# Optimization experiments

Hardware: AMD Instinct MI355X
Metric: run time of the kernel (lower is better)

Reference implementation:

```python
import jax, jax.numpy as jnp
import numpy as np

NUM_BINS = 10
NUM_CLASSES = 128
ALPHA = 0.999
LABEL_SMOOTHING = 0.0


def setup_inputs() -> dict:
    key = jax.random.key(0)
    k1, k2, k3 = jax.random.split(key, 3)
    B, T, C = 16, 4096, NUM_CLASSES
    return {
        "pred_logits": jax.random.normal(k1, (B, T, C), dtype=jnp.float32),
        "target_prob": jax.random.uniform(k2, (B, T, C), dtype=jnp.float32),
        "mask": jax.random.uniform(k3, (B, T, 1), dtype=jnp.float32),
        "GD_stat_ema": jnp.ones((NUM_BINS,), dtype=jnp.float32),
        "label_stat_ema_each_class": jnp.ones((NUM_CLASSES * 3,), dtype=jnp.float32),
    }


def _bce_with_logits(x, t):
    # numerically stable BCEWithLogitsLoss, reduction='none'
    return jnp.maximum(x, 0.0) - x * t + jnp.log1p(jnp.exp(-jnp.abs(x)))


def _update_ema(ema, hist, num_bins):
    hist = hist / jnp.maximum(hist.sum(), 1e-10) * num_bins
    ema = ema * ALPHA + (1.0 - ALPHA) * hist
    return ema / jnp.maximum(ema.sum(), 1e-10) * num_bins


def reference(pred_logits, target_prob, mask, GD_stat_ema, label_stat_ema_each_class):
    m = jnp.broadcast_to(mask, pred_logits.shape)
    tp = jnp.clip(target_prob, LABEL_SMOOTHING, 1.0 - LABEL_SMOOTHING)

    raw_loss = _bce_with_logits(pred_logits, tp)
    pred_prob = jax.nn.sigmoid(pred_logits)
    grad_mag = jnp.abs(pred_prob - tp)

    bin_idx = jnp.clip(jnp.floor(grad_mag * NUM_BINS).astype(jnp.int32), 0, NUM_BINS - 1)
    GD_weights = 1.0 / jax.lax.stop_gradient(GD_stat_ema[bin_idx])

    # per-class 3-way probability bin: idx in [0, 3*num_classes)
    tpi = jnp.clip(jnp.floor(tp * 3.0).astype(jnp.int32), 0, 2) + 3 * jnp.arange(NUM_CLASSES, dtype=jnp.int32)
    classes_weights = 1.0 / jax.lax.stop_gradient(label_stat_ema_each_class[tpi])

    weights = jnp.sqrt(GD_weights * classes_weights)
    loss = (raw_loss * weights * m).sum() / jnp.maximum(m.sum(), 1e-10)

    # weighted histograms (bincount with float weights)
    GD_hist = jnp.zeros((NUM_BINS,), dtype=jnp.float32).at[bin_idx.ravel()].add(m.ravel())
    label_hist = jnp.zeros((NUM_CLASSES * 3,), dtype=jnp.float32).at[tpi.ravel()].add(m.ravel())

    GD_ema_new = _update_ema(GD_stat_ema, GD_hist, NUM_BINS)
    label_ema_new = _update_ema(label_stat_ema_each_class, label_hist, NUM_CLASSES * 3)
    return loss, GD_ema_new, label_ema_new
```

## Files before the change

kernel.cpp:

```cpp
#include <hip/hip_runtime.h>

#define NBINS 10
#define LBINS 384
#define NOUT  395
#define PSTRIDE 400
#define PQ (PSTRIDE / 4)
#define BLOCK 256

typedef float f32x4 __attribute__((ext_vector_type(4)));

#define SGRID 1024
#define OUTER 2
#define BATCH 4
#define SGSTR (SGRID * BLOCK)

__global__ __launch_bounds__(256) void ghm_main_s(
    const float* __restrict__ xg, const float* __restrict__ tg,
    const float* __restrict__ mask,
    const float* __restrict__ gd_ema, const float* __restrict__ lab_ema,
    float* __restrict__ ws)
{
    __shared__ float s_rsgd[NBINS];
    __shared__ float s_rslab[LBINS];
    __shared__ float s_out[PSTRIDE];
    __shared__ float s_red[4];

    const int tid = threadIdx.x;
    if (tid < NBINS) s_rsgd[tid] = __builtin_amdgcn_rsqf(gd_ema[tid]);
    for (int i = tid; i < LBINS; i += BLOCK) s_rslab[i] = __builtin_amdgcn_rsqf(lab_ema[i]);
    for (int i = tid; i < PSTRIDE; i += BLOCK) s_out[i] = 0.f;
    __syncthreads();

    const int c0 = (tid & 31) * 4;
    float wl[4][3];
#pragma unroll
    for (int j = 0; j < 4; ++j)
#pragma unroll
        for (int t = 0; t < 3; ++t) wl[j][t] = s_rslab[(c0 + j) * 3 + t];

    float lab[4][3] = {{0.f}};
    float gdl[NBINS];
#pragma unroll
    for (int b = 0; b < NBINS; ++b) gdl[b] = 0.f;
    float loss_acc = 0.f;

    const f32x4* x4 = (const f32x4*)xg;
    const f32x4* t4 = (const f32x4*)tg;
    const int i0 = blockIdx.x * BLOCK + tid;

#pragma unroll
    for (int o = 0; o < OUTER; ++o) {
        f32x4 xv[BATCH], tv[BATCH]; float mv[BATCH];
#pragma unroll
        for (int k = 0; k < BATCH; ++k) {
            const int i = i0 + (o * BATCH + k) * SGSTR;
            xv[k] = __builtin_nontemporal_load(&x4[i]);
            tv[k] = __builtin_nontemporal_load(&t4[i]);
            mv[k] = __builtin_nontemporal_load(&mask[i >> 5]);
        }
#pragma unroll
        for (int k = 0; k < BATCH; ++k) {
            const float m = mv[k];
            const float xs[4] = {xv[k].x, xv[k].y, xv[k].z, xv[k].w};
            const float ts[4] = {tv[k].x, tv[k].y, tv[k].z, tv[k].w};
            unsigned pack = 0u;
#pragma unroll
            for (int j = 0; j < 4; ++j) {
                const float x  = xs[j];
                const float tp = ts[j];
                const float E  = __expf(-fabsf(x));
                const float z  = 1.f + E;
                const float raw = fmaxf(x, 0.f) - x * tp + __logf(z);
                const float inv = __builtin_amdgcn_rcpf(z);
                const float tps = (x >= 0.f) ? tp : 1.f - tp;
                const float g   = fabsf(inv - tps);
                int bin = (int)(g * 10.f);  bin = bin > 9 ? 9 : bin;
                int t3  = (int)(tp * 3.f);  t3  = t3 > 2 ? 2 : t3;
                const float wlj = (t3 == 0) ? wl[j][0] : ((t3 == 1) ? wl[j][1] : wl[j][2]);
                const float w = s_rsgd[bin] * wlj;
                loss_acc = fmaf(raw * m, w, loss_acc);
#pragma unroll
                for (int t = 0; t < 3; ++t) lab[j][t] += (t3 == t) ? m : 0.f;
                pack += 1u << (3 * bin);
            }
#pragma unroll
            for (int b = 0; b < NBINS; ++b)
                gdl[b] = fmaf(m, (float)((pack >> (3 * b)) & 7u), gdl[b]);
        }
    }

    const int lane = tid & 63, wv = tid >> 6;
    float v = loss_acc;
#pragma unroll
    for (int off = 32; off > 0; off >>= 1) v += __shfl_down(v, off);
    if (lane == 0) s_red[wv] = v;
#pragma unroll
    for (int b = 0; b < NBINS; ++b) {
        float g = gdl[b];
#pragma unroll
        for (int off = 32; off > 0; off >>= 1) g += __shfl_down(g, off);
        if (lane == 0) atomicAdd(&s_out[1 + b], g);
    }
#pragma unroll
    for (int j = 0; j < 4; ++j)
#pragma unroll
        for (int t = 0; t < 3; ++t)
            atomicAdd(&s_out[11 + (c0 + j) * 3 + t], lab[j][t]);
    __syncthreads();

    float* slot = ws + (size_t)blockIdx.x * PSTRIDE;
    if (tid == 0) slot[0] = s_red[0] + s_red[1] + s_red[2] + s_red[3];
    if (tid >= 1) slot[tid] = s_out[tid];
    if (tid < PSTRIDE - BLOCK) slot[BLOCK + tid] = s_out[BLOCK + tid];
}

__global__ __launch_bounds__(256) void ghm_fin1(
    const float* __restrict__ ws, float* __restrict__ ws2, int nrows)
{
    __shared__ float4 r[BLOCK];
    const int tid = threadIdx.x;
    const float4* p = (const float4*)ws + blockIdx.x;
    float4 a = make_float4(0.f, 0.f, 0.f, 0.f);
    for (int b = tid; b < nrows; b += BLOCK) {
        float4 u = p[(size_t)b * PQ];
        a.x += u.x; a.y += u.y; a.z += u.z; a.w += u.w;
    }
    r[tid] = a;
    __syncthreads();
    for (int off = BLOCK / 2; off > 0; off >>= 1) {
        if (tid < off) {
            float4 u = r[tid + off];
            r[tid].x += u.x; r[tid].y += u.y; r[tid].z += u.z; r[tid].w += u.w;
        }
        __syncthreads();
    }
    if (tid == 0) ((float4*)ws2)[blockIdx.x] = r[0];
}

__global__ __launch_bounds__(512) void ghm_fin2(
    const float* __restrict__ sv_g,
    const float* __restrict__ gd_ema, const float* __restrict__ lab_ema,
    float* __restrict__ out)
{
    __shared__ float sv[PSTRIDE];
    __shared__ float red[512];
    __shared__ float s_sc[1];

    const int tid = threadIdx.x;
    if (tid < PSTRIDE) sv[tid] = sv_g[tid];
    __syncthreads();

    if (tid == 0) {
        float ms = 0.f;
        for (int b = 0; b < NBINS; ++b) ms += sv[1 + b];
        const float inv_m = 1.f / fmaxf(ms, 1e-10f);
        s_sc[0] = inv_m;
        out[0] = sv[0] * inv_m;
        float ge[NBINS], gs = 0.f;
        for (int b = 0; b < NBINS; ++b) {
            ge[b] = gd_ema[b] * 0.999f + 0.001f * (sv[1 + b] * inv_m * (float)NBINS);
            gs += ge[b];
        }
        const float ig = 1.f / fmaxf(gs, 1e-10f);
        for (int b = 0; b < NBINS; ++b) out[1 + b] = ge[b] * ig * (float)NBINS;
    }
    __syncthreads();
    const float inv_m = s_sc[0];

    float e = 0.f;
    if (tid < LBINS)
        e = lab_ema[tid] * 0.999f + 0.001f * (sv[11 + tid] * inv_m * (float)LBINS);
    red[tid] = e;
    __syncthreads();
    for (int off = 256; off > 0; off >>= 1) {
        if (tid < off) red[tid] += red[tid + off];
        __syncthreads();
    }
    const float ie = (float)LBINS / fmaxf(red[0], 1e-10f);
    if (tid < LBINS) out[11 + tid] = e * ie;
}

#define NSLICE 8
#define SLICE_STRIDE 512
#define AGRID 2048
#define AITER 4
#define AGSTR (AGRID * BLOCK)

__global__ __launch_bounds__(256) void ghm_main_a(
    const float* __restrict__ xg, const float* __restrict__ tg,
    const float* __restrict__ mask,
    const float* __restrict__ gd_ema, const float* __restrict__ lab_ema,
    float* __restrict__ ws)
{
    __shared__ float s_rsgd[NBINS];
    __shared__ float s_rslab[LBINS];
    __shared__ float s_hlab[LBINS];
    __shared__ float s_hgd[NBINS];
    __shared__ float s_red[4];

    const int tid = threadIdx.x;
    if (tid < NBINS) { s_rsgd[tid] = __builtin_amdgcn_rsqf(gd_ema[tid]); s_hgd[tid] = 0.f; }
    for (int i = tid; i < LBINS; i += BLOCK) {
        s_rslab[i] = __builtin_amdgcn_rsqf(lab_ema[i]);
        s_hlab[i]  = 0.f;
    }
    __syncthreads();

    const int c0 = (tid & 31) * 4;
    float wl[4][3];
#pragma unroll
    for (int j = 0; j < 4; ++j)
#pragma unroll
        for (int t = 0; t < 3; ++t) wl[j][t] = s_rslab[(c0 + j) * 3 + t];

    float lab[4][3] = {{0.f}};
    float gdl[NBINS];
#pragma unroll
    for (int b = 0; b < NBINS; ++b) gdl[b] = 0.f;
    float loss_acc = 0.f;

    const float4* x4 = (const float4*)xg;
    const float4* t4 = (const float4*)tg;
    const int i0 = blockIdx.x * BLOCK + tid;

    float4 xv[AITER], tv[AITER]; float mv[AITER];
#pragma unroll
    for (int k = 0; k < AITER; ++k) {
        const int i = i0 + k * AGSTR;
        xv[k] = x4[i]; tv[k] = t4[i]; mv[k] = mask[i >> 5];
    }
#pragma unroll
    for (int k = 0; k < AITER; ++k) {
        const float m = mv[k];
        const float xs[4] = {xv[k].x, xv[k].y, xv[k].z, xv[k].w};
        const float ts[4] = {tv[k].x, tv[k].y, tv[k].z, tv[k].w};
        unsigned pack = 0u;
#pragma unroll
        for (int j = 0; j < 4; ++j) {
            const float x  = xs[j];
            const float tp = ts[j];
            const float E  = __expf(-fabsf(x));
            const float z  = 1.f + E;
            const float raw = fmaxf(x, 0.f) - x * tp + __logf(z);
            const float inv = __builtin_amdgcn_rcpf(z);
            const float tps = (x >= 0.f) ? tp : 1.f - tp;
            const float g   = fabsf(inv - tps);
            int bin = (int)(g * 10.f);  bin = bin > 9 ? 9 : bin;
            int t3  = (int)(tp * 3.f);  t3  = t3 > 2 ? 2 : t3;
            const float wlj = (t3 == 0) ? wl[j][0] : ((t3 == 1) ? wl[j][1] : wl[j][2]);
            const float w = s_rsgd[bin] * wlj;
            loss_acc = fmaf(raw * m, w, loss_acc);
#pragma unroll
            for (int t = 0; t < 3; ++t) lab[j][t] += (t3 == t) ? m : 0.f;
            pack += 1u << (3 * bin);
        }
#pragma unroll
        for (int b = 0; b < NBINS; ++b)
            gdl[b] = fmaf(m, (float)((pack >> (3 * b)) & 7u), gdl[b]);
    }

    const int lane = tid & 63, wv = tid >> 6;
    float v = loss_acc;
#pragma unroll
    for (int off = 32; off > 0; off >>= 1) v += __shfl_down(v, off);
    if (lane == 0) s_red[wv] = v;
#pragma unroll
    for (int b = 0; b < NBINS; ++b) {
        float g = gdl[b];
#pragma unroll
        for (int off = 32; off > 0; off >>= 1) g += __shfl_down(g, off);
        if (lane == 0) atomicAdd(&s_hgd[b], g);
    }
#pragma unroll
    for (int j = 0; j < 4; ++j)
#pragma unroll
        for (int t = 0; t < 3; ++t)
            atomicAdd(&s_hlab[(c0 + j) * 3 + t], lab[j][t]);
    __syncthreads();

    float* wss = ws + (blockIdx.x & (NSLICE - 1)) * SLICE_STRIDE;
    if (tid == 0) atomicAdd(&wss[0], s_red[0] + s_red[1] + s_red[2] + s_red[3]);
    if (tid < NBINS) atomicAdd(&wss[1 + tid], s_hgd[tid]);
    for (int e = tid; e < LBINS; e += BLOCK) atomicAdd(&wss[1 + NBINS + e], s_hlab[e]);
}

__global__ __launch_bounds__(512) void ghm_fin_a(
    const float* __restrict__ ws,
    const float* __restrict__ gd_ema, const float* __restrict__ lab_ema,
    float* __restrict__ out)
{
    __shared__ float red[512];
    __shared__ float s_gde[NBINS];
    __shared__ float s_gesum;

    const int tid = threadIdx.x;
    float v = 0.f;
    if (tid < NOUT) {
#pragma unroll
        for (int s = 0; s < NSLICE; ++s) v += ws[s * SLICE_STRIDE + tid];
    }
    red[tid] = (tid >= 1 && tid < 1 + NBINS) ? v : 0.f;
    __syncthreads();
    for (int off = 256; off > 0; off >>= 1) {
        if (tid < off) red[tid] += red[tid + off];
        __syncthreads();
    }
    const float msum = red[0];
    __syncthreads();
    const float inv_m = 1.f / fmaxf(msum, 1e-10f);
    if (tid == 0) out[0] = v * inv_m;
    if (tid >= 1 && tid < 1 + NBINS) {
        float hn = v * inv_m * (float)NBINS;
        s_gde[tid - 1] = gd_ema[tid - 1] * 0.999f + 0.001f * hn;
    }
    __syncthreads();
    if (tid == 0) {
        float s = 0.f;
        for (int b = 0; b < NBINS; ++b) s += s_gde[b];
        s_gesum = s;
    }
    __syncthreads();
    if (tid >= 1 && tid < 1 + NBINS)
        out[tid] = s_gde[tid - 1] / fmaxf(s_gesum, 1e-10f) * (float)NBINS;

    float e = 0.f;
    if (tid >= 1 + NBINS && tid < NOUT) {
        float hn = v * inv_m * (float)LBINS;
        e = lab_ema[tid - 1 - NBINS] * 0.999f + 0.001f * hn;
    }
    red[tid] = e;
    __syncthreads();
    for (int off = 256; off > 0; off >>= 1) {
        if (tid < off) red[tid] += red[tid + off];
        __syncthreads();
    }
    const float esum = red[0];
    if (tid >= 1 + NBINS && tid < NOUT)
        out[tid] = e / fmaxf(esum, 1e-10f) * (float)LBINS;
}

extern "C" void kernel_launch(void* const* d_in, const int* in_sizes, int n_in,
                              void* d_out, int out_size, void* d_ws, size_t ws_size,
                              hipStream_t stream)
{
    const float* logits  = (const float*)d_in[0];
    const float* tprob   = (const float*)d_in[1];
    const float* mask    = (const float*)d_in[2];
    const float* gd_ema  = (const float*)d_in[3];
    const float* lab_ema = (const float*)d_in[4];
    float* out = (float*)d_out;
    float* ws  = (float*)d_ws;

    const size_t need_s = ((size_t)SGRID * PSTRIDE + PSTRIDE) * sizeof(float);
    if (ws_size >= need_s) {
        float* ws2 = ws + (size_t)SGRID * PSTRIDE;
        ghm_main_s<<<SGRID, BLOCK, 0, stream>>>(logits, tprob, mask, gd_ema, lab_ema, ws);
        ghm_fin1<<<PQ, BLOCK, 0, stream>>>(ws, ws2, SGRID);
        ghm_fin2<<<1, 512, 0, stream>>>(ws2, gd_ema, lab_ema, out);
    } else {
        hipMemsetAsync(ws, 0, NSLICE * SLICE_STRIDE * sizeof(float), stream);
        ghm_main_a<<<AGRID, BLOCK, 0, stream>>>(logits, tprob, mask, gd_ema, lab_ema, ws);
        ghm_fin_a<<<1, 512, 0, stream>>>(ws, gd_ema, lab_ema, out);
    }
}
```

Before: 142.3 us.

## Stream inputs through LDS with direct global-to-LDS loads and staged waits

The main kernel now issues all eight iterations' logits and target loads up front as global_load_lds transfers into a 64KB per-block LDS pipeline buffer. Each stage waits on a decreasing vmcnt so compute on early tiles overlaps the remaining loads. The per-element math is factored into a shared helper that the fallback kernel also uses. The large LDS allocation lowers occupancy, and the nontemporal load hints are dropped.

```diff
diff --git a/kernel.cpp b/kernel.cpp
--- a/kernel.cpp
+++ b/kernel.cpp
@@ -9,12 +9,45 @@
 
 typedef float f32x4 __attribute__((ext_vector_type(4)));
 
+#define TO_LDS(p) ((__attribute__((address_space(3))) void*)(uintptr_t)(p))
+#define TO_GLB(p) ((const __attribute__((address_space(1))) void*)(uintptr_t)(p))
+
 #define SGRID 1024
-#define OUTER 2
-#define BATCH 4
 #define SGSTR (SGRID * BLOCK)
 
-__global__ __launch_bounds__(256) void ghm_main_s(
+__device__ __forceinline__ void ghm_elem4(
+    const f32x4 xv, const f32x4 tv, const float m,
+    const float wl[4][3], const float* s_rsgd,
+    float lab[4][3], float gdl[NBINS], float& loss_acc)
+{
+    const float xs[4] = {xv.x, xv.y, xv.z, xv.w};
+    const float ts[4] = {tv.x, tv.y, tv.z, tv.w};
+    unsigned pack = 0u;
+#pragma unroll
+    for (int j = 0; j < 4; ++j) {
+        const float x  = xs[j];
+        const float tp = ts[j];
+        const float E  = __expf(-fabsf(x));
+        const float z  = 1.f + E;
+        const float raw = fmaxf(x, 0.f) - x * tp + __logf(z);
+        const float inv = __builtin_amdgcn_rcpf(z);
+        const float tps = (x >= 0.f) ? tp : 1.f - tp;
+        const float g   = fabsf(inv - tps);
+        int bin = (int)(g * 10.f);  bin = bin > 9 ? 9 : bin;
+        int t3  = (int)(tp * 3.f);  t3  = t3 > 2 ? 2 : t3;
+        const float wlj = (t3 == 0) ? wl[j][0] : ((t3 == 1) ? wl[j][1] : wl[j][2]);
+        const float w = s_rsgd[bin] * wlj;
+        loss_acc = fmaf(raw * m, w, loss_acc);
+#pragma unroll
+        for (int t = 0; t < 3; ++t) lab[j][t] += (t3 == t) ? m : 0.f;
+        pack += 1u << (3 * bin);
+    }
+#pragma unroll
+    for (int b = 0; b < NBINS; ++b)
+        gdl[b] = fmaf(m, (float)((pack >> (3 * b)) & 7u), gdl[b]);
+}
+
+__global__ __launch_bounds__(256) void ghm_main_l(
     const float* __restrict__ xg, const float* __restrict__ tg,
     const float* __restrict__ mask,
     const float* __restrict__ gd_ema, const float* __restrict__ lab_ema,
@@ -24,6 +57,7 @@
     __shared__ float s_rslab[LBINS];
     __shared__ float s_out[PSTRIDE];
     __shared__ float s_red[4];
+    __shared__ __align__(16) float s_pipe[4][8][2][256];
 
     const int tid = threadIdx.x;
     if (tid < NBINS) s_rsgd[tid] = __builtin_amdgcn_rsqf(gd_ema[tid]);
@@ -46,50 +80,33 @@
 
     const f32x4* x4 = (const f32x4*)xg;
     const f32x4* t4 = (const f32x4*)tg;
+    const int lane = tid & 63, wv = tid >> 6;
     const int i0 = blockIdx.x * BLOCK + tid;
 
-#pragma unroll
-    for (int o = 0; o < OUTER; ++o) {
-        f32x4 xv[BATCH], tv[BATCH]; float mv[BATCH];
-#pragma unroll
-        for (int k = 0; k < BATCH; ++k) {
-            const int i = i0 + (o * BATCH + k) * SGSTR;
-            xv[k] = __builtin_nontemporal_load(&x4[i]);
-            tv[k] = __builtin_nontemporal_load(&t4[i]);
-            mv[k] = __builtin_nontemporal_load(&mask[i >> 5]);
-        }
-#pragma unroll
-        for (int k = 0; k < BATCH; ++k) {
-            const float m = mv[k];
-            const float xs[4] = {xv[k].x, xv[k].y, xv[k].z, xv[k].w};
-            const float ts[4] = {tv[k].x, tv[k].y, tv[k].z, tv[k].w};
-            unsigned pack = 0u;
-#pragma unroll
-            for (int j = 0; j < 4; ++j) {
-                const float x  = xs[j];
-                const float tp = ts[j];
-                const float E  = __expf(-fabsf(x));
-                const float z  = 1.f + E;
-                const float raw = fmaxf(x, 0.f) - x * tp + __logf(z);
-                const float inv = __builtin_amdgcn_rcpf(z);
-                const float tps = (x >= 0.f) ? tp : 1.f - tp;
-                const float g   = fabsf(inv - tps);
-                int bin = (int)(g * 10.f);  bin = bin > 9 ? 9 : bin;
-                int t3  = (int)(tp * 3.f);  t3  = t3 > 2 ? 2 : t3;
-                const float wlj = (t3 == 0) ? wl[j][0] : ((t3 == 1) ? wl[j][1] : wl[j][2]);
-                const float w = s_rsgd[bin] * wlj;
-                loss_acc = fmaf(raw * m, w, loss_acc);
-#pragma unroll
-                for (int t = 0; t < 3; ++t) lab[j][t] += (t3 == t) ? m : 0.f;
-                pack += 1u << (3 * bin);
-            }
-#pragma unroll
-            for (int b = 0; b < NBINS; ++b)
-                gdl[b] = fmaf(m, (float)((pack >> (3 * b)) & 7u), gdl[b]);
-        }
-    }
-
-    const int lane = tid & 63, wv = tid >> 6;
+    float mv[8];
+#pragma unroll
+    for (int k = 0; k < 8; ++k) mv[k] = mask[(i0 + k * SGSTR) >> 5];
+#pragma unroll
+    for (int k = 0; k < 8; ++k) asm volatile("" : "+v"(mv[k]));
+
+#pragma unroll
+    for (int k = 0; k < 8; ++k) {
+        const int i = i0 + k * SGSTR;
+        __builtin_amdgcn_global_load_lds(TO_GLB(x4 + i), TO_LDS(&s_pipe[wv][k][0][0]), 16, 0, 0);
+        __builtin_amdgcn_global_load_lds(TO_GLB(t4 + i), TO_LDS(&s_pipe[wv][k][1][0]), 16, 0, 0);
+    }
+
+#define GHM_STAGE(K, NW) do {                                                 \
+        asm volatile("s_waitcnt vmcnt(" #NW ")" ::: "memory");                \
+        const f32x4 xv = *(const f32x4*)&s_pipe[wv][K][0][lane * 4];          \
+        const f32x4 tv = *(const f32x4*)&s_pipe[wv][K][1][lane * 4];          \
+        ghm_elem4(xv, tv, mv[K], wl, s_rsgd, lab, gdl, loss_acc);             \
+    } while (0)
+
+    GHM_STAGE(0, 14); GHM_STAGE(1, 12); GHM_STAGE(2, 10); GHM_STAGE(3, 8);
+    GHM_STAGE(4, 6);  GHM_STAGE(5, 4);  GHM_STAGE(6, 2);  GHM_STAGE(7, 0);
+#undef GHM_STAGE
+
     float v = loss_acc;
 #pragma unroll
     for (int off = 32; off > 0; off >>= 1) v += __shfl_down(v, off);
@@ -219,45 +236,19 @@
     for (int b = 0; b < NBINS; ++b) gdl[b] = 0.f;
     float loss_acc = 0.f;
 
-    const float4* x4 = (const float4*)xg;
-    const float4* t4 = (const float4*)tg;
+    const f32x4* x4 = (const f32x4*)xg;
+    const f32x4* t4 = (const f32x4*)tg;
     const int i0 = blockIdx.x * BLOCK + tid;
 
-    float4 xv[AITER], tv[AITER]; float mv[AITER];
+    f32x4 xv[AITER], tv[AITER]; float mv[AITER];
 #pragma unroll
     for (int k = 0; k < AITER; ++k) {
         const int i = i0 + k * AGSTR;
         xv[k] = x4[i]; tv[k] = t4[i]; mv[k] = mask[i >> 5];
     }
 #pragma unroll
-    for (int k = 0; k < AITER; ++k) {
-        const float m = mv[k];
-        const float xs[4] = {xv[k].x, xv[k].y, xv[k].z, xv[k].w};
-        const float ts[4] = {tv[k].x, tv[k].y, tv[k].z, tv[k].w};
-        unsigned pack = 0u;
-#pragma unroll
-        for (int j = 0; j < 4; ++j) {
-            const float x  = xs[j];
-            const float tp = ts[j];
-            const float E  = __expf(-fabsf(x));
-            const float z  = 1.f + E;
-            const float raw = fmaxf(x, 0.f) - x * tp + __logf(z);
-            const float inv = __builtin_amdgcn_rcpf(z);
-            const float tps = (x >= 0.f) ? tp : 1.f - tp;
-            const float g   = fabsf(inv - tps);
-            int bin = (int)(g * 10.f);  bin = bin > 9 ? 9 : bin;
-            int t3  = (int)(tp * 3.f);  t3  = t3 > 2 ? 2 : t3;
-            const float wlj = (t3 == 0) ? wl[j][0] : ((t3 == 1) ? wl[j][1] : wl[j][2]);
-            const float w = s_rsgd[bin] * wlj;
-            loss_acc = fmaf(raw * m, w, loss_acc);
-#pragma unroll
-            for (int t = 0; t < 3; ++t) lab[j][t] += (t3 == t) ? m : 0.f;
-            pack += 1u << (3 * bin);
-        }
-#pragma unroll
-        for (int b = 0; b < NBINS; ++b)
-            gdl[b] = fmaf(m, (float)((pack >> (3 * b)) & 7u), gdl[b]);
-    }
+    for (int k = 0; k < AITER; ++k)
+        ghm_elem4(xv[k], tv[k], mv[k], wl, s_rsgd, lab, gdl, loss_acc);
 
     const int lane = tid & 63, wv = tid >> 6;
     float v = loss_acc;
@@ -351,10 +342,10 @@
     float* out = (float*)d_out;
     float* ws  = (float*)d_ws;
 
-    const size_t need_s = ((size_t)SGRID * PSTRIDE + PSTRIDE) * sizeof(float);
-    if (ws_size >= need_s) {
+    const size_t need = ((size_t)SGRID * PSTRIDE + PSTRIDE) * sizeof(float);
+    if (ws_size >= need) {
         float* ws2 = ws + (size_t)SGRID * PSTRIDE;
-        ghm_main_s<<<SGRID, BLOCK, 0, stream>>>(logits, tprob, mask, gd_ema, lab_ema, ws);
+        ghm_main_l<<<SGRID, BLOCK, 0, stream>>>(logits, tprob, mask, gd_ema, lab_ema, ws);
         ghm_fin1<<<PQ, BLOCK, 0, stream>>>(ws, ws2, SGRID);
         ghm_fin2<<<1, 512, 0, stream>>>(ws2, gd_ema, lab_ema, out);
     } else {
```

Result: no change. 141.4 us (-0.6%).
